# Optimization experiments

Hardware: AMD Instinct MI355X
Metric: run time of the kernel (lower is better)

## Reference

```python
import jax, jax.numpy as jnp
import numpy as np

# Faithful RBF layer math:
# dists[n,k] = sum_d relu(sigma[d]) * (x[n,d]-center[k,d])^2  (original builds an NxN
# matrix per center just to take its diagonal; we use the algebraic expansion
# x^2.s - 2 (x*s).c^T + c^2.s which is O(N*K*D) and identical math)
# D2 = 1 - dists * relu(width); concat bias column of ones; out = D2_bias @ relu(W_out)

N, D, K, OUT = 131072, 256, 256, 128

def setup_inputs() -> dict:
    key = jax.random.key(0)
    k1, k2, k3, k4 = jax.random.split(key, 4)
    x = jax.random.normal(k1, (N, D), dtype=jnp.float32)
    # 'uniform' keras initializer ~ U(-0.05, 0.05)
    center = jax.random.uniform(k2, (K, D), minval=-0.05, maxval=0.05, dtype=jnp.float32)
    sigma = jax.random.uniform(k3, (1, D), minval=0.5, maxval=1.0, dtype=jnp.float32)
    width = jnp.ones((1, K), dtype=jnp.float32)
    output_weights = jax.random.uniform(k4, (1 + K, OUT), minval=0.5, maxval=1.0, dtype=jnp.float32)
    return {"x": x, "center": center, "sigma": sigma, "width": width,
            "output_weights": output_weights}

def reference(x, center, sigma, width, output_weights):
    s = jax.nn.relu(sigma[0])                       # [D]
    x2 = (x * x) @ s                                # [N]
    c2 = (center * center) @ s                      # [K]
    cross = (x * s) @ center.T                      # [N,K]
    dists = x2[:, None] - 2.0 * cross + c2[None, :] # [N,K] weighted sq-dists
    D2 = 1.0 - dists * jax.nn.relu(width)           # [N,K]
    ones = jnp.ones((x.shape[0], 1), dtype=x.dtype)
    D2_bias = jnp.concatenate([ones, D2], axis=1)   # [N,1+K]
    return D2_bias @ jax.nn.relu(output_weights)    # [N,OUT]
```

## Files before the change

kernel.cpp:

```cpp
#include <hip/hip_runtime.h>


typedef short  short8 __attribute__((ext_vector_type(8)));
typedef __bf16 bf16x8 __attribute__((ext_vector_type(8)));
typedef float  f32x4  __attribute__((ext_vector_type(4)));

#define N_ 131072
#define D_ 256
#define K_ 256
#define O_ 128

__device__ __forceinline__ unsigned short f2bf_bits(float f) {
  unsigned u = __builtin_bit_cast(unsigned, f);
  u += 0x7fffu + ((u >> 16) & 1u);
  return (unsigned short)(u >> 16);
}

__device__ __forceinline__ float relu(float v) { return v > 0.f ? v : 0.f; }

__global__ __launch_bounds__(256) void rbf_pre(
    const float* __restrict__ center, const float* __restrict__ sigma,
    const float* __restrict__ width,  const float* __restrict__ W,
    short* __restrict__ Mfrag, float* __restrict__ Bo, float* __restrict__ S1)
{
  const int tid = threadIdx.x;
  if (blockIdx.x < 64) {
    const int ot = blockIdx.x & 7;
    const int ks = blockIdx.x >> 3;
    __shared__ float ww[K_][16];
    __shared__ float cen[K_][32];
#pragma unroll
    for (int i = 0; i < 16; ++i) {
      const int k  = i * 16 + (tid >> 4);
      const int oc = tid & 15;
      ww[k][oc] = relu(width[k]) * relu(W[(1 + k) * O_ + ot * 16 + oc]);
    }
#pragma unroll
    for (int i = 0; i < 32; ++i) {
      const int k  = i * 8 + (tid >> 5);
      const int dc = tid & 31;
      cen[k][dc] = center[k * D_ + ks * 32 + dc];
    }
    __syncthreads();
    const int j   = tid & 7;
    const int lf  = tid >> 3;
    const int oc  = lf & 15;
    const int dc1 = (lf >> 4) * 8 + j;
    float a1 = 0.f, a2 = 0.f;
#pragma unroll 8
    for (int k = 0; k < K_; ++k) {
      const float w = ww[k][oc];
      a1 = fmaf(cen[k][dc1],      w, a1);
      a2 = fmaf(cen[k][dc1 + 16], w, a2);
    }
    const int e1 = blockIdx.x * 512 + tid;
    const int d1 = ks * 32 + dc1;
    Mfrag[e1]       = (short)f2bf_bits(a1 * relu(sigma[d1]));
    Mfrag[e1 + 256] = (short)f2bf_bits(a2 * relu(sigma[d1 + 16]));
  } else {
    __shared__ float c2s[K_];
    {
      const f32x4* cr = (const f32x4*)(center + tid * D_);
      const f32x4* sr = (const f32x4*)sigma;
      f32x4 acc = {0.f, 0.f, 0.f, 0.f};
#pragma unroll 8
      for (int d4 = 0; d4 < D_ / 4; ++d4) {
        const f32x4 c = cr[d4];
        const f32x4 s = sr[d4];
#pragma unroll
        for (int e = 0; e < 4; ++e) acc[e] = fmaf(c[e] * c[e], relu(s[e]), acc[e]);
      }
      c2s[tid] = (acc[0] + acc[1]) + (acc[2] + acc[3]);
    }
    __syncthreads();
    if (tid < O_) {
      const int o = tid;
      float s1 = 0.f, sum = 0.f, c2w = 0.f;
#pragma unroll 4
      for (int k = 0; k < K_; ++k) {
        const float w  = relu(width[k]);
        const float wr = relu(W[(1 + k) * O_ + o]);
        s1  = fmaf(w, wr, s1);
        sum += wr;
        c2w = fmaf(c2s[k] * w, wr, c2w);
      }
      Bo[o] = relu(W[o]) + sum - c2w;
      S1[o] = s1;
    }
  }
}

__global__ __launch_bounds__(512, 2) void rbf_main(
    const float* __restrict__ x, const float* __restrict__ sigma,
    const short* __restrict__ Mfrag, const float* __restrict__ Bo,
    const float* __restrict__ S1, float* __restrict__ out)
{
  __shared__ short8 Blds[4096];
  const int tid  = threadIdx.x;
  const int lane = tid & 63;
  const int wv   = tid >> 6;
  const int m    = lane & 15;
  const int q    = lane >> 4;
  const long rowBase = ((long)blockIdx.x * 8 + wv) * 16;

  short8 stg[8];
  const short8* Mf8 = (const short8*)Mfrag;
#pragma unroll
  for (int i = 0; i < 8; ++i) stg[i] = Mf8[i * 512 + tid];

  const float* xr = x + (rowBase + m) * D_ + q * 8;
  f32x4 raw[16];
#pragma unroll
  for (int ks = 0; ks < 8; ++ks) {
    raw[2 * ks]     = *(const f32x4*)(xr + ks * 32);
    raw[2 * ks + 1] = *(const f32x4*)(xr + ks * 32 + 4);
  }

#pragma unroll
  for (int i = 0; i < 8; ++i) Blds[i * 512 + tid] = stg[i];

  const float* sp = sigma + q * 8;
  bf16x8 a[8];
  float x2 = 0.f;
#pragma unroll
  for (int ks = 0; ks < 8; ++ks) {
    float sv[8], v[8];
    *(f32x4*)(sv)     = *(const f32x4*)(sp + ks * 32);
    *(f32x4*)(sv + 4) = *(const f32x4*)(sp + ks * 32 + 4);
    *(f32x4*)(v)      = raw[2 * ks];
    *(f32x4*)(v + 4)  = raw[2 * ks + 1];
    short8 ab;
#pragma unroll
    for (int jj = 0; jj < 8; ++jj) {
      const float s = relu(sv[jj]);
      x2 = fmaf(s * v[jj], v[jj], x2);
      ab[jj] = (short)f2bf_bits(v[jj]);
    }
    a[ks] = __builtin_bit_cast(bf16x8, ab);
  }
  x2 += __shfl_xor(x2, 16);
  x2 += __shfl_xor(x2, 32);

  __syncthreads();

#pragma unroll
  for (int ot = 0; ot < 8; ++ot) {
    f32x4 acc = {0.f, 0.f, 0.f, 0.f};
#pragma unroll
    for (int ks = 0; ks < 8; ++ks) {
      const bf16x8 bb =
          __builtin_bit_cast(bf16x8, Blds[(ks * 8 + ot) * 64 + lane]);
      acc = __builtin_amdgcn_mfma_f32_16x16x32_bf16(a[ks], bb, acc, 0, 0, 0);
    }
    const int   o  = ot * 16 + m;
    const float bo = Bo[o];
    const float s1 = S1[o];
    float* op = out + rowBase * O_ + o;
#pragma unroll
    for (int r = 0; r < 4; ++r) {
      const int rr = q * 4 + r;
      const float x2r = __shfl(x2, rr);
      op[(long)rr * O_] = fmaf(2.f, acc[r], fmaf(-x2r, s1, bo));
    }
  }
}

extern "C" void kernel_launch(void* const* d_in, const int* in_sizes, int n_in,
                              void* d_out, int out_size, void* d_ws, size_t ws_size,
                              hipStream_t stream) {
  (void)in_sizes; (void)n_in; (void)out_size; (void)ws_size;
  const float* x      = (const float*)d_in[0];
  const float* center = (const float*)d_in[1];
  const float* sigma  = (const float*)d_in[2];
  const float* width  = (const float*)d_in[3];
  const float* W      = (const float*)d_in[4];
  float* out = (float*)d_out;

  short* Mfrag = (short*)d_ws;
  float* Bo    = (float*)((char*)d_ws + 65536);
  float* S1    = (float*)((char*)d_ws + 66048);

  hipLaunchKernelGGL(rbf_pre, dim3(65), dim3(256), 0, stream,
                     center, sigma, width, W, Mfrag, Bo, S1);
  hipLaunchKernelGGL(rbf_main, dim3(1024), dim3(512), 0, stream,
                     x, sigma, Mfrag, Bo, S1, out);
}
```

Baseline: 250.6 us.

## Process two row tiles per wave to amortize B-fragment LDS staging

Halves the grid so each wave handles two 16-row tiles, one in each half of the rows. The LDS copy of the bf16 weight matrix is loaded once and reused for both tiles. Both tiles' x rows are loaded up front to raise memory-level parallelism. It also precomputes relu(sigma) in the pre-kernel and stages sigma, Bo and S1 in LDS so the per-row loops avoid global loads. The cost is higher register pressure from holding two raw x buffers, plus fewer blocks to spread across the GPU.

```diff
diff --git a/kernel.cpp b/kernel.cpp
--- a/kernel.cpp
+++ b/kernel.cpp
@@ -21,7 +21,8 @@
 __global__ __launch_bounds__(256) void rbf_pre(
     const float* __restrict__ center, const float* __restrict__ sigma,
     const float* __restrict__ width,  const float* __restrict__ W,
-    short* __restrict__ Mfrag, float* __restrict__ Bo, float* __restrict__ S1)
+    short* __restrict__ Mfrag, float* __restrict__ Bo, float* __restrict__ S1,
+    float* __restrict__ SR)
 {
   const int tid = threadIdx.x;
   if (blockIdx.x < 64) {
@@ -59,6 +60,7 @@
     Mfrag[e1 + 256] = (short)f2bf_bits(a2 * relu(sigma[d1 + 16]));
   } else {
     __shared__ float c2s[K_];
+    SR[tid] = relu(sigma[tid]);
     {
       const f32x4* cr = (const f32x4*)(center + tid * D_);
       const f32x4* sr = (const f32x4*)sigma;
@@ -91,78 +93,102 @@
 }
 
 __global__ __launch_bounds__(512, 2) void rbf_main(
-    const float* __restrict__ x, const float* __restrict__ sigma,
-    const short* __restrict__ Mfrag, const float* __restrict__ Bo,
+    const float* __restrict__ x, const short* __restrict__ Mfrag,
+    const float* __restrict__ SR, const float* __restrict__ Bo,
     const float* __restrict__ S1, float* __restrict__ out)
 {
   __shared__ short8 Blds[4096];
+  __shared__ float  sigL[256];
+  __shared__ float  BoL[128];
+  __shared__ float  S1L[128];
+
   const int tid  = threadIdx.x;
   const int lane = tid & 63;
   const int wv   = tid >> 6;
   const int m    = lane & 15;
   const int q    = lane >> 4;
-  const long rowBase = ((long)blockIdx.x * 8 + wv) * 16;
-
-  short8 stg[8];
-  const short8* Mf8 = (const short8*)Mfrag;
-#pragma unroll
-  for (int i = 0; i < 8; ++i) stg[i] = Mf8[i * 512 + tid];
-
-  const float* xr = x + (rowBase + m) * D_ + q * 8;
-  f32x4 raw[16];
+
+  {
+    const short8* Mf8 = (const short8*)Mfrag;
+    short8 stg[8];
+#pragma unroll
+    for (int i = 0; i < 8; ++i) stg[i] = Mf8[i * 512 + tid];
+#pragma unroll
+    for (int i = 0; i < 8; ++i) Blds[i * 512 + tid] = stg[i];
+    if (tid < 64)       ((f32x4*)sigL)[tid]     = ((const f32x4*)SR)[tid];
+    else if (tid < 96)  ((f32x4*)BoL)[tid - 64] = ((const f32x4*)Bo)[tid - 64];
+    else if (tid < 128) ((f32x4*)S1L)[tid - 96] = ((const f32x4*)S1)[tid - 96];
+  }
+  __syncthreads();
+
+  const long t0 = (long)blockIdx.x * 8 + wv;
+  const long r0 = t0 * 16;
+  const long r1 = (t0 + 4096) * 16;
+  const float* xr0 = x + (r0 + m) * D_ + q * 8;
+  const float* xr1 = x + (r1 + m) * D_ + q * 8;
+
+  f32x4 raw0[16], raw1[16];
 #pragma unroll
   for (int ks = 0; ks < 8; ++ks) {
-    raw[2 * ks]     = *(const f32x4*)(xr + ks * 32);
-    raw[2 * ks + 1] = *(const f32x4*)(xr + ks * 32 + 4);
-  }
-
-#pragma unroll
-  for (int i = 0; i < 8; ++i) Blds[i * 512 + tid] = stg[i];
-
-  const float* sp = sigma + q * 8;
-  bf16x8 a[8];
-  float x2 = 0.f;
+    raw0[2 * ks]     = *(const f32x4*)(xr0 + ks * 32);
+    raw0[2 * ks + 1] = *(const f32x4*)(xr0 + ks * 32 + 4);
+  }
 #pragma unroll
   for (int ks = 0; ks < 8; ++ks) {
-    float sv[8], v[8];
-    *(f32x4*)(sv)     = *(const f32x4*)(sp + ks * 32);
-    *(f32x4*)(sv + 4) = *(const f32x4*)(sp + ks * 32 + 4);
-    *(f32x4*)(v)      = raw[2 * ks];
-    *(f32x4*)(v + 4)  = raw[2 * ks + 1];
-    short8 ab;
-#pragma unroll
-    for (int jj = 0; jj < 8; ++jj) {
-      const float s = relu(sv[jj]);
-      x2 = fmaf(s * v[jj], v[jj], x2);
-      ab[jj] = (short)f2bf_bits(v[jj]);
-    }
-    a[ks] = __builtin_bit_cast(bf16x8, ab);
-  }
-  x2 += __shfl_xor(x2, 16);
-  x2 += __shfl_xor(x2, 32);
-
-  __syncthreads();
-
+    raw1[2 * ks]     = *(const f32x4*)(xr1 + ks * 32);
+    raw1[2 * ks + 1] = *(const f32x4*)(xr1 + ks * 32 + 4);
+  }
+
+  float bo8[8], s18[8];
 #pragma unroll
   for (int ot = 0; ot < 8; ++ot) {
-    f32x4 acc = {0.f, 0.f, 0.f, 0.f};
+    bo8[ot] = BoL[ot * 16 + m];
+    s18[ot] = S1L[ot * 16 + m];
+  }
+
+  auto process = [&](const f32x4 (&raw)[16], long rowBase) {
+    bf16x8 a[8];
+    float x2 = 0.f;
 #pragma unroll
     for (int ks = 0; ks < 8; ++ks) {
-      const bf16x8 bb =
-          __builtin_bit_cast(bf16x8, Blds[(ks * 8 + ot) * 64 + lane]);
-      acc = __builtin_amdgcn_mfma_f32_16x16x32_bf16(a[ks], bb, acc, 0, 0, 0);
-    }
-    const int   o  = ot * 16 + m;
-    const float bo = Bo[o];
-    const float s1 = S1[o];
-    float* op = out + rowBase * O_ + o;
-#pragma unroll
-    for (int r = 0; r < 4; ++r) {
-      const int rr = q * 4 + r;
-      const float x2r = __shfl(x2, rr);
-      op[(long)rr * O_] = fmaf(2.f, acc[r], fmaf(-x2r, s1, bo));
-    }
-  }
+      float sv[8], v[8];
+      *(f32x4*)(sv)     = *(const f32x4*)(sigL + ks * 32 + q * 8);
+      *(f32x4*)(sv + 4) = *(const f32x4*)(sigL + ks * 32 + q * 8 + 4);
+      *(f32x4*)(v)      = raw[2 * ks];
+      *(f32x4*)(v + 4)  = raw[2 * ks + 1];
+      short8 ab;
+#pragma unroll
+      for (int jj = 0; jj < 8; ++jj) {
+        x2 = fmaf(sv[jj] * v[jj], v[jj], x2);
+        ab[jj] = (short)f2bf_bits(v[jj]);
+      }
+      a[ks] = __builtin_bit_cast(bf16x8, ab);
+    }
+    x2 += __shfl_xor(x2, 16);
+    x2 += __shfl_xor(x2, 32);
+    float xb[4];
+#pragma unroll
+    for (int r = 0; r < 4; ++r) xb[r] = __shfl(x2, q * 4 + r);
+
+#pragma unroll
+    for (int ot = 0; ot < 8; ++ot) {
+      f32x4 acc = {0.f, 0.f, 0.f, 0.f};
+#pragma unroll
+      for (int ks = 0; ks < 8; ++ks) {
+        const bf16x8 bb =
+            __builtin_bit_cast(bf16x8, Blds[(ks * 8 + ot) * 64 + lane]);
+        acc = __builtin_amdgcn_mfma_f32_16x16x32_bf16(a[ks], bb, acc, 0, 0, 0);
+      }
+      float* op = out + rowBase * O_ + ot * 16 + m;
+#pragma unroll
+      for (int r = 0; r < 4; ++r)
+        op[(long)(q * 4 + r) * O_] =
+            fmaf(2.f, acc[r], fmaf(-xb[r], s18[ot], bo8[ot]));
+    }
+  };
+
+  process(raw0, r0);
+  process(raw1, r1);
 }
 
 extern "C" void kernel_launch(void* const* d_in, const int* in_sizes, int n_in,
@@ -179,9 +205,10 @@
   short* Mfrag = (short*)d_ws;
   float* Bo    = (float*)((char*)d_ws + 65536);
   float* S1    = (float*)((char*)d_ws + 66048);
+  float* SR    = (float*)((char*)d_ws + 66560);
 
   hipLaunchKernelGGL(rbf_pre, dim3(65), dim3(256), 0, stream,
-                     center, sigma, width, W, Mfrag, Bo, S1);
-  hipLaunchKernelGGL(rbf_main, dim3(1024), dim3(512), 0, stream,
-                     x, sigma, Mfrag, Bo, S1, out);
-}
+                     center, sigma, width, W, Mfrag, Bo, S1, SR);
+  hipLaunchKernelGGL(rbf_main, dim3(512), dim3(512), 0, stream,
+                     x, Mfrag, SR, Bo, S1, out);
+}
```

New measurement: 251.7 us. About the same (+0.4%).
